# Performance work log

Hardware: AMD Instinct MI355X
Metric: run time of the kernel (lower is better)

The kernel has to match this reference:

```python
import jax, jax.numpy as jnp
import numpy as np

N_NODES = 20000
N_EDGES = 320000
D = 128  # d_edge = d_node = d_global


def setup_inputs() -> dict:
    key = jax.random.key(0)
    ks = jax.random.split(key, 8)
    inv = lambda fan_in: 1.0 / np.sqrt(fan_in)
    return {
        "edge_attr": jax.random.normal(ks[0], (N_EDGES, D), dtype=jnp.float32),
        "node_attr": jax.random.normal(ks[1], (N_NODES, D), dtype=jnp.float32),
        "u": jax.random.normal(ks[2], (D,), dtype=jnp.float32),
        "senders": jax.random.randint(ks[3], (N_EDGES,), 0, N_NODES, dtype=jnp.int32),
        "receivers": jax.random.randint(ks[4], (N_EDGES,), 0, N_NODES, dtype=jnp.int32),
        "We": jax.random.normal(ks[5], (4 * D, D), dtype=jnp.float32) * inv(4 * D),
        "be": jnp.zeros((D,), dtype=jnp.float32),
        "Wv": jax.random.normal(ks[6], (3 * D, D), dtype=jnp.float32) * inv(3 * D),
        "bv": jnp.zeros((D,), dtype=jnp.float32),
        "Wu": jax.random.normal(ks[7], (3 * D, D), dtype=jnp.float32) * inv(3 * D),
        "bu": jnp.zeros((D,), dtype=jnp.float32),
    }


def reference(edge_attr, node_attr, u, senders, receivers, We, be, Wv, bv, Wu, bu):
    E = edge_attr.shape[0]
    N = node_attr.shape[0]
    u_e = jnp.broadcast_to(u, (E, u.shape[0]))
    u_v = jnp.broadcast_to(u, (N, u.shape[0]))

    # Edge block: phi_e(e, v_r, v_s, u) -- gather endpoint features per edge
    e_in = jnp.concatenate(
        [edge_attr, node_attr[receivers], node_attr[senders], u_e], axis=-1
    )  # [E, 4D]
    e_new = jax.nn.relu(e_in @ We + be)  # [E, D]

    # rho_ev: sum incoming edges per receiver node (scatter-add)
    aggr_e = jax.ops.segment_sum(e_new, receivers, num_segments=N)  # [N, D]

    # Node block: phi_v(aggr_e, v, u)
    v_in = jnp.concatenate([aggr_e, node_attr, u_v], axis=-1)  # [N, 3D]
    v_new = jax.nn.relu(v_in @ Wv + bv)  # [N, D]

    # Global block: rho_eu / rho_vu = mean, phi_u(aggr_e, aggr_v, u)
    aggr_e_u = jnp.mean(e_new, axis=0)
    aggr_v_u = jnp.mean(v_new, axis=0)
    u_in = jnp.concatenate([aggr_e_u, aggr_v_u, u], axis=-1)  # [3D]
    u_new = jax.nn.relu(u_in @ Wu + bu)  # [D]

    return e_new, v_new, u_new
```

## Files before the change

### kernel.cpp

```cpp
#include <hip/hip_runtime.h>
#include <hip/hip_bf16.h>


#define NN 20000
#define NE 320000
#define DD 128
#define SAS 136
#define SBS 136
#define NBLK 512
#define NTILE 5000

#define BAR_LDS() asm volatile("s_waitcnt lgkmcnt(0)\n\ts_barrier" ::: "memory")

typedef unsigned short u16;
typedef __attribute__((ext_vector_type(8))) short bf16x8;
typedef __attribute__((ext_vector_type(4))) float f32x4;

__device__ __forceinline__ float b2f(unsigned short h) {
  return __uint_as_float(((unsigned int)h) << 16);
}
__device__ __forceinline__ unsigned short f2b(float f) {
  unsigned int u = __float_as_uint(f);
  unsigned int r = (u + 0x7fffu + ((u >> 16) & 1u)) >> 16;
  return (unsigned short)r;
}
__device__ __forceinline__ unsigned int addpk(unsigned int a, unsigned int b) {
  float lo = __uint_as_float(a << 16) + __uint_as_float(b << 16);
  float hi = __uint_as_float(a & 0xffff0000u) + __uint_as_float(b & 0xffff0000u);
  return (unsigned int)f2b(lo) | (((unsigned int)f2b(hi)) << 16);
}

__device__ __forceinline__ void mfma_core(const u16* sA, const u16* sBT,
                                          int lane, int w, f32x4 acc[4][2]) {
  int r15 = lane & 15;
  int koff = (lane >> 4) * 8;
#pragma unroll
  for (int k0 = 0; k0 < DD; k0 += 32) {
    bf16x8 a[4], b[2];
#pragma unroll
    for (int mt = 0; mt < 4; ++mt)
      a[mt] = *(const bf16x8*)&sA[(mt * 16 + r15) * SAS + k0 + koff];
#pragma unroll
    for (int nt = 0; nt < 2; ++nt)
      b[nt] = *(const bf16x8*)&sBT[(w * 32 + nt * 16 + r15) * SBS + k0 + koff];
#pragma unroll
    for (int mt = 0; mt < 4; ++mt)
#pragma unroll
      for (int nt = 0; nt < 2; ++nt)
        acc[mt][nt] = __builtin_amdgcn_mfma_f32_16x16x32_bf16(
            a[mt], b[nt], acc[mt][nt], 0, 0, 0);
  }
}

__device__ __forceinline__ void stage_w(u16* sBT, const u16* wsrc, int tid) {
  const uint4* ws = (const uint4*)wsrc;
  for (int i = tid; i < DD * DD / 8; i += 256) {
    int n = i >> 4, kk = (i & 15) * 8;
    *(uint4*)&sBT[n * SBS + kk] = ws[i];
  }
}

__global__ __launch_bounds__(256) void k_setup(const int* recv, int* counts,
                                               const float* We, const float* Wv,
                                               const float* u, const float* be,
                                               const float* bv, u16* wt,
                                               float* ce, float* cv) {
  __shared__ float su[DD];
  int b = blockIdx.x, tid = threadIdx.x;
  if (b < 1250) {
    atomicAdd(&counts[recv[b * 256 + tid]], 1);
  } else if (b < 1255) {
    int m = b - 1250;
    const float* W = (m == 0)   ? We
                     : (m == 1) ? We + 128 * DD
                     : (m == 2) ? We + 256 * DD
                     : (m == 3) ? Wv + 128 * DD
                                : Wv;
    u16* o = wt + (size_t)m * DD * DD;
    for (int i = tid; i < DD * DD; i += 256) {
      int k = i >> 7, n = i & 127;
      o[n * DD + k] = f2b(W[i]);
    }
  } else {
    if (tid < DD) su[tid] = u[tid];
    __syncthreads();
    if (tid < DD) {
      float a = be[tid], c = bv[tid];
      for (int k = 0; k < DD; ++k) {
        a = fmaf(su[k], We[(384 + k) * DD + tid], a);
        c = fmaf(su[k], Wv[(256 + k) * DD + tid], c);
      }
      ce[tid] = a;
      cv[tid] = c;
    }
  }
}

__global__ void k_scan(const int* counts, int* rowptr, int* cursor) {
  __shared__ int wsum[16];
  __shared__ int carry;
  int tid = threadIdx.x;
  int lane = tid & 63, wv = tid >> 6;
  if (tid == 0) carry = 0;
  __syncthreads();
  for (int base = 0; base < NN; base += 1024) {
    int i = base + tid;
    int v = (i < NN) ? counts[i] : 0;
    int x = v;
    for (int off = 1; off < 64; off <<= 1) {
      int t = __shfl_up(x, off);
      if (lane >= off) x += t;
    }
    if (lane == 63) wsum[wv] = x;
    __syncthreads();
    if (wv == 0 && lane < 16) {
      int y = wsum[lane];
      for (int off = 1; off < 16; off <<= 1) {
        int t = __shfl_up(y, off);
        if (lane >= off) y += t;
      }
      wsum[lane] = y;
    }
    __syncthreads();
    int woff = (wv > 0) ? wsum[wv - 1] : 0;
    int excl = carry + woff + (x - v);
    if (i < NN) {
      rowptr[i] = excl;
      cursor[i] = excl;
    }
    __syncthreads();
    if (tid == 0) carry += wsum[15];
    __syncthreads();
  }
  if (tid == 0) rowptr[NN] = carry;
}

__global__ __launch_bounds__(256) void k_mid(const int* recv, int* cursor,
                                             int* elist, const float* node_attr,
                                             const u16* wt, u16* P) {
  __shared__ __align__(16) u16 sA[64 * SAS];
  __shared__ __align__(16) u16 sBT[DD * SBS];
  int b = blockIdx.x, tid = threadIdx.x;
  if (b < 1250) {
    int e = b * 256 + tid;
    int slot = atomicAdd(&cursor[recv[e]], 1);
    elist[slot] = e;
    return;
  }
  int g = b - 1250;
  int n0 = (g / 3) * 64;
  int sel = g % 3;
  stage_w(sBT, wt + (size_t)(1 + sel) * DD * DD, tid);
  for (int i = tid; i < 64 * DD / 4; i += 256) {
    int rr = i >> 5, cc = (i & 31) * 4;
    float4 a4 = (n0 + rr < NN)
                    ? ((const float4*)node_attr)[(size_t)(n0 + rr) * 32 + (i & 31)]
                    : make_float4(0, 0, 0, 0);
    ushort4 h;
    h.x = f2b(a4.x); h.y = f2b(a4.y); h.z = f2b(a4.z); h.w = f2b(a4.w);
    *(ushort4*)&sA[rr * SAS + cc] = h;
  }
  __syncthreads();
  int lane = tid & 63, w = tid >> 6;
  int c15 = lane & 15, quad = lane >> 4;
  int col0 = w * 32 + c15, col1 = col0 + 16;
  f32x4 acc[4][2] = {};
  mfma_core(sA, sBT, lane, w, acc);
#pragma unroll
  for (int mt = 0; mt < 4; ++mt)
#pragma unroll
    for (int r = 0; r < 4; ++r) {
      int n = n0 + mt * 16 + quad * 4 + r;
      if (n < NN) {
        u16* o = &P[(size_t)n * 384 + sel * 128];
        o[col0] = f2b(acc[mt][0][r]);
        o[col1] = f2b(acc[mt][1][r]);
      }
    }
}

__global__ __launch_bounds__(512, 4) void k_edge(const float* edge_attr,
                                                 const u16* wt, const int* elist,
                                                 const int* recv, const int* send,
                                                 const u16* P, const float* ce,
                                                 float* e_out, float* aggr,
                                                 float* sum_e) {
  __shared__ __align__(16) u16 sA[64 * SAS];
  __shared__ __align__(16) u16 sPQ[64 * SAS];
  __shared__ int sEid[64], sRecv[64], sSend[64];
  int tid = threadIdx.x;
  int lane = tid & 63, w = tid >> 6;
  int r15 = lane & 15, quad = lane >> 4;
  int koff = quad * 8;
  int col0 = w * 16 + r15;
  int myrow = tid >> 5;
  int mycol = (tid & 31) * 4;
  int grow = tid >> 4;
  int gch = tid & 15;

  bf16x8 breg[4];
#pragma unroll
  for (int kk = 0; kk < 4; ++kk)
    breg[kk] =
        *(const bf16x8*)&wt[(size_t)(w * 16 + r15) * DD + kk * 32 + koff];
  float ce0 = ce[col0];

  float4 areg[4];
  int eid4[4];
  int eidN = 0, rcN = 0, sdN = 0;
  int t = blockIdx.x;

  {
    int base = t * 64;
#pragma unroll
    for (int j = 0; j < 4; ++j) eid4[j] = elist[base + myrow + 16 * j];
    if (tid < 64) {
      eidN = elist[base + tid];
      rcN = recv[eidN];
      sdN = send[eidN];
    }
#pragma unroll
    for (int j = 0; j < 4; ++j)
      areg[j] = *(const float4*)&edge_attr[(size_t)eid4[j] * DD + mycol];
  }
  float colsum = 0.f;
  bool first = true;

  for (; t < NTILE; t += NBLK) {
    if (!first) BAR_LDS();
    first = false;
#pragma unroll
    for (int j = 0; j < 4; ++j) {
      ushort4 h;
      h.x = f2b(areg[j].x); h.y = f2b(areg[j].y);
      h.z = f2b(areg[j].z); h.w = f2b(areg[j].w);
      *(ushort4*)&sA[(myrow + 16 * j) * SAS + mycol] = h;
    }
    if (tid < 64) {
      sEid[tid] = eidN;
      sRecv[tid] = rcN;
      sSend[tid] = sdN;
    }
    BAR_LDS();

    uint4 q1[2], q2[2];
#pragma unroll
    for (int j = 0; j < 2; ++j) {
      int row = grow + 32 * j;
      q1[j] = *((const uint4*)&P[(size_t)sRecv[row] * 384] + gch);
      q2[j] = *((const uint4*)&P[(size_t)sSend[row] * 384 + 128] + gch);
    }
    int tn = t + NBLK;
    if (tn < NTILE) {
      int base = tn * 64;
#pragma unroll
      for (int j = 0; j < 4; ++j) eid4[j] = elist[base + myrow + 16 * j];
      if (tid < 64) eidN = elist[base + tid];
    }

    f32x4 acc[4] = {};
#pragma unroll
    for (int kk = 0; kk < 4; ++kk) {
      bf16x8 a[4];
#pragma unroll
      for (int mt = 0; mt < 4; ++mt)
        a[mt] = *(const bf16x8*)&sA[(mt * 16 + r15) * SAS + kk * 32 + koff];
#pragma unroll
      for (int mt = 0; mt < 4; ++mt)
        acc[mt] = __builtin_amdgcn_mfma_f32_16x16x32_bf16(a[mt], breg[kk],
                                                          acc[mt], 0, 0, 0);
    }
    if (tn < NTILE) {
      if (tid < 64) {
        rcN = recv[eidN];
        sdN = send[eidN];
      }
#pragma unroll
      for (int j = 0; j < 4; ++j)
        areg[j] = *(const float4*)&edge_attr[(size_t)eid4[j] * DD + mycol];
    }
#pragma unroll
    for (int j = 0; j < 2; ++j) {
      int row = grow + 32 * j;
      uint4 o;
      o.x = addpk(q1[j].x, q2[j].x);
      o.y = addpk(q1[j].y, q2[j].y);
      o.z = addpk(q1[j].z, q2[j].z);
      o.w = addpk(q1[j].w, q2[j].w);
      *(uint4*)&sPQ[row * SAS + gch * 8] = o;
    }
    BAR_LDS();

#pragma unroll
    for (int mt = 0; mt < 4; ++mt)
#pragma unroll
      for (int r = 0; r < 4; ++r) {
        int m = mt * 16 + quad * 4 + r;
        float v = fmaxf(acc[mt][r] + b2f(sPQ[m * SAS + col0]) + ce0, 0.f);
        sA[m * SAS + col0] = f2b(v);
      }
    BAR_LDS();

    if (tid < 256) {
      int col = tid & 127, half = tid >> 7;
      int r0 = half * 32;
      float run = 0.f;
      int prev = sRecv[r0];
      for (int r = r0; r < r0 + 32; ++r) {
        int cur = sRecv[r];
        float v = b2f(sA[r * SAS + col]);
        if (cur != prev) {
          atomicAdd(&aggr[(size_t)prev * DD + col], run);
          run = 0.f;
          prev = cur;
        }
        run += v;
        colsum += v;
      }
      atomicAdd(&aggr[(size_t)prev * DD + col], run);
    } else {
      int tt = tid - 256;
#pragma unroll
      for (int j = 0; j < 4; ++j) {
        int i = tt + 256 * j;
        int row = i >> 4, ch = (i & 15) * 8;
        uint4 qq = *(const uint4*)&sA[row * SAS + ch];
        float4 f0, f1;
        f0.x = b2f((u16)(qq.x & 0xffff)); f0.y = b2f((u16)(qq.x >> 16));
        f0.z = b2f((u16)(qq.y & 0xffff)); f0.w = b2f((u16)(qq.y >> 16));
        f1.x = b2f((u16)(qq.z & 0xffff)); f1.y = b2f((u16)(qq.z >> 16));
        f1.z = b2f((u16)(qq.w & 0xffff)); f1.w = b2f((u16)(qq.w >> 16));
        float* dst = &e_out[(size_t)sEid[row] * DD + ch];
        *(float4*)dst = f0;
        *(float4*)(dst + 4) = f1;
      }
    }
  }
  if (tid < 256) atomicAdd(&sum_e[tid & 127], colsum);
}

__global__ __launch_bounds__(256) void k_node(const float* aggr, const u16* wt,
                                              const u16* P, const float* cv,
                                              float* v_out, float* sum_v) {
  __shared__ __align__(16) u16 sA[64 * SAS];
  __shared__ __align__(16) u16 sBT[DD * SBS];
  __shared__ float sCol[DD];
  int tid = threadIdx.x;
  int n0 = blockIdx.x * 64;
  stage_w(sBT, wt + (size_t)4 * DD * DD, tid);
  for (int i = tid; i < 64 * DD / 4; i += 256) {
    int rr = i >> 5, cc = (i & 31) * 4;
    float4 a4 = (n0 + rr < NN)
                    ? ((const float4*)aggr)[(size_t)(n0 + rr) * 32 + (i & 31)]
                    : make_float4(0, 0, 0, 0);
    ushort4 h;
    h.x = f2b(a4.x); h.y = f2b(a4.y); h.z = f2b(a4.z); h.w = f2b(a4.w);
    *(ushort4*)&sA[rr * SAS + cc] = h;
  }
  if (tid < DD) sCol[tid] = 0.f;
  __syncthreads();
  int lane = tid & 63, w = tid >> 6;
  f32x4 acc[4][2] = {};
  mfma_core(sA, sBT, lane, w, acc);
  int c15 = lane & 15, quad = lane >> 4;
  int col0 = w * 32 + c15, col1 = col0 + 16;
  float cv0 = cv[col0], cv1 = cv[col1];
  float cs0 = 0.f, cs1 = 0.f;
#pragma unroll
  for (int mt = 0; mt < 4; ++mt)
#pragma unroll
    for (int r = 0; r < 4; ++r) {
      int n = n0 + mt * 16 + quad * 4 + r;
      if (n < NN) {
        const u16* pv = &P[(size_t)n * 384 + 256];
        float v0 = fmaxf(acc[mt][0][r] + b2f(pv[col0]) + cv0, 0.f);
        float v1 = fmaxf(acc[mt][1][r] + b2f(pv[col1]) + cv1, 0.f);
        size_t ob = (size_t)n * DD;
        v_out[ob + col0] = v0;
        v_out[ob + col1] = v1;
        cs0 += v0;
        cs1 += v1;
      }
    }
  atomicAdd(&sCol[col0], cs0);
  atomicAdd(&sCol[col1], cs1);
  __syncthreads();
  if (tid < DD) atomicAdd(&sum_v[tid], sCol[tid]);
}

__global__ void k_global(const float* sumbuf, const float* u, const float* Wu,
                         const float* bu, float* out) {
  __shared__ float sin_[384];
  int j = threadIdx.x;
  sin_[j] = sumbuf[j] * (1.0f / (float)NE);
  sin_[128 + j] = sumbuf[128 + j] * (1.0f / (float)NN);
  sin_[256 + j] = u[j];
  __syncthreads();
  float a = bu[j];
  for (int k = 0; k < 384; ++k) a = fmaf(sin_[k], Wu[k * DD + j], a);
  out[j] = fmaxf(a, 0.f);
}

extern "C" void kernel_launch(void* const* d_in, const int* in_sizes, int n_in,
                              void* d_out, int out_size, void* d_ws,
                              size_t ws_size, hipStream_t stream) {
  const float* edge_attr = (const float*)d_in[0];
  const float* node_attr = (const float*)d_in[1];
  const float* u = (const float*)d_in[2];
  const int* senders = (const int*)d_in[3];
  const int* receivers = (const int*)d_in[4];
  const float* We = (const float*)d_in[5];
  const float* be = (const float*)d_in[6];
  const float* Wv = (const float*)d_in[7];
  const float* bv = (const float*)d_in[8];
  const float* Wu = (const float*)d_in[9];
  const float* bu = (const float*)d_in[10];

  float* e_out = (float*)d_out;
  float* v_out = e_out + (size_t)NE * DD;
  float* u_out = v_out + (size_t)NN * DD;

  int* counts = (int*)d_ws;
  float* sumbuf = (float*)d_ws + NN;
  float* aggr = (float*)d_ws + NN + 256;
  int* rowptr = (int*)d_ws + NN + 256 + NN * DD;
  int* cursor = rowptr + NN + 1;
  int* elist = cursor + NN;
  size_t off = (size_t)(NN + 256 + NN * DD + (NN + 1) + NN + NE);
  off = (off + 3) & ~(size_t)3;
  u16* wt = (u16*)((float*)d_ws + off);
  u16* P = wt + (size_t)5 * DD * DD;
  float* ce = (float*)(P + (size_t)NN * 384);
  float* cv = ce + 128;

  hipMemsetAsync(d_ws, 0, (size_t)(NN + 256 + NN * DD) * 4, stream);
  k_setup<<<1256, 256, 0, stream>>>(receivers, counts, We, Wv, u, be, bv, wt,
                                    ce, cv);
  k_scan<<<1, 1024, 0, stream>>>(counts, rowptr, cursor);
  k_mid<<<1250 + 939, 256, 0, stream>>>(receivers, cursor, elist, node_attr,
                                        wt, P);
  k_edge<<<NBLK, 512, 0, stream>>>(edge_attr, wt, elist, receivers, senders, P,
                                   ce, e_out, aggr, sumbuf);
  k_node<<<(NN + 63) / 64, 256, 0, stream>>>(aggr, wt, P, cv, v_out,
                                             sumbuf + 128);
  k_global<<<1, 128, 0, stream>>>(sumbuf, u, Wu, bu, u_out);
}
```

Measured before the change: 494.5 us.

## Deepen edge-kernel prefetch pipeline with double-buffered metadata and early P gathers

The edge kernel now keeps edge indices, receiver/sender metadata and the gathered P rows one or two tiles ahead, using double-buffered shared arrays for per-tile metadata. This way the dependent index→recv/send→P gather chain is spread across iterations instead of stalling inside one. The setup kernel's weight transpose now goes through shared memory so the global stores are coalesced. The barrier macro also switches to the builtin barrier. In exchange, more registers stay live across iterations, which may cut occupancy under the 512-thread launch bound.

```diff
diff --git a/kernel.cpp b/kernel.cpp
--- a/kernel.cpp
+++ b/kernel.cpp
@@ -10,7 +10,11 @@
 #define NBLK 512
 #define NTILE 5000
 
-#define BAR_LDS() asm volatile("s_waitcnt lgkmcnt(0)\n\ts_barrier" ::: "memory")
+#define BAR_LDS()                                        \
+  do {                                                   \
+    asm volatile("s_waitcnt lgkmcnt(0)" ::: "memory");   \
+    __builtin_amdgcn_s_barrier();                        \
+  } while (0)
 
 typedef unsigned short u16;
 typedef __attribute__((ext_vector_type(8))) short bf16x8;
@@ -66,6 +70,7 @@
                                                const float* bv, u16* wt,
                                                float* ce, float* cv) {
   __shared__ float su[DD];
+  __shared__ __align__(16) u16 sT[DD * SAS];
   int b = blockIdx.x, tid = threadIdx.x;
   if (b < 1250) {
     atomicAdd(&counts[recv[b * 256 + tid]], 1);
@@ -76,10 +81,15 @@
                      : (m == 2) ? We + 256 * DD
                      : (m == 3) ? Wv + 128 * DD
                                 : Wv;
-    u16* o = wt + (size_t)m * DD * DD;
     for (int i = tid; i < DD * DD; i += 256) {
       int k = i >> 7, n = i & 127;
-      o[n * DD + k] = f2b(W[i]);
+      sT[n * SAS + k] = f2b(W[i]);
+    }
+    __syncthreads();
+    u16* o = wt + (size_t)m * DD * DD;
+    for (int i = tid; i < DD * DD / 8; i += 256) {
+      int n = i >> 4, c = (i & 15) * 8;
+      *(uint4*)&o[n * DD + c] = *(const uint4*)&sT[n * SAS + c];
     }
   } else {
     if (tid < DD) su[tid] = u[tid];
@@ -187,7 +197,7 @@
                                                  float* sum_e) {
   __shared__ __align__(16) u16 sA[64 * SAS];
   __shared__ __align__(16) u16 sPQ[64 * SAS];
-  __shared__ int sEid[64], sRecv[64], sSend[64];
+  __shared__ int sEid[2][64], sRecv[2][64], sSend[2][64];
   int tid = threadIdx.x;
   int lane = tid & 63, w = tid >> 6;
   int r15 = lane & 15, quad = lane >> 4;
@@ -206,27 +216,49 @@
   float ce0 = ce[col0];
 
   float4 areg[4];
-  int eid4[4];
-  int eidN = 0, rcN = 0, sdN = 0;
+  int eid4R[4];
+  int metaE = 0, metaRc = 0, metaSd = 0;
+  int eidNN = 0;
+  uint4 q1[2], q2[2];
+
   int t = blockIdx.x;
-
   {
     int base = t * 64;
-#pragma unroll
-    for (int j = 0; j < 4; ++j) eid4[j] = elist[base + myrow + 16 * j];
     if (tid < 64) {
-      eidN = elist[base + tid];
-      rcN = recv[eidN];
-      sdN = send[eidN];
-    }
+      int e = elist[base + tid];
+      metaE = e; metaRc = recv[e]; metaSd = send[e];
+      sEid[0][tid] = e; sRecv[0][tid] = metaRc; sSend[0][tid] = metaSd;
+    }
+#pragma unroll
+    for (int j = 0; j < 4; ++j) eid4R[j] = elist[base + myrow + 16 * j];
 #pragma unroll
     for (int j = 0; j < 4; ++j)
-      areg[j] = *(const float4*)&edge_attr[(size_t)eid4[j] * DD + mycol];
+      areg[j] = *(const float4*)&edge_attr[(size_t)eid4R[j] * DD + mycol];
+    BAR_LDS();
+#pragma unroll
+    for (int j = 0; j < 2; ++j) {
+      int row = grow + 32 * j;
+      q1[j] = *((const uint4*)&P[(size_t)sRecv[0][row] * 384] + gch);
+      q2[j] = *((const uint4*)&P[(size_t)sSend[0][row] * 384 + 128] + gch);
+    }
+    int tn = t + NBLK;
+    if (tn < NTILE) {
+      int bn = tn * 64;
+#pragma unroll
+      for (int j = 0; j < 4; ++j) eid4R[j] = elist[bn + myrow + 16 * j];
+      if (tid < 64) {
+        int e = elist[bn + tid];
+        metaE = e; metaRc = recv[e]; metaSd = send[e];
+      }
+    }
   }
   float colsum = 0.f;
+  int cur = 0;
   bool first = true;
 
   for (; t < NTILE; t += NBLK) {
+    int tn = t + NBLK, tnn = tn + NBLK;
+    int nxt = cur ^ 1;
     if (!first) BAR_LDS();
     first = false;
 #pragma unroll
@@ -236,27 +268,23 @@
       h.z = f2b(areg[j].z); h.w = f2b(areg[j].w);
       *(ushort4*)&sA[(myrow + 16 * j) * SAS + mycol] = h;
     }
-    if (tid < 64) {
-      sEid[tid] = eidN;
-      sRecv[tid] = rcN;
-      sSend[tid] = sdN;
+    if (tn < NTILE) {
+#pragma unroll
+      for (int j = 0; j < 4; ++j)
+        areg[j] = *(const float4*)&edge_attr[(size_t)eid4R[j] * DD + mycol];
+    }
+    if (tnn < NTILE) {
+      int bn = tnn * 64;
+#pragma unroll
+      for (int j = 0; j < 4; ++j) eid4R[j] = elist[bn + myrow + 16 * j];
+      if (tid < 64) eidNN = elist[bn + tid];
+    }
+    if (tn < NTILE && tid < 64) {
+      sEid[nxt][tid] = metaE;
+      sRecv[nxt][tid] = metaRc;
+      sSend[nxt][tid] = metaSd;
     }
     BAR_LDS();
-
-    uint4 q1[2], q2[2];
-#pragma unroll
-    for (int j = 0; j < 2; ++j) {
-      int row = grow + 32 * j;
-      q1[j] = *((const uint4*)&P[(size_t)sRecv[row] * 384] + gch);
-      q2[j] = *((const uint4*)&P[(size_t)sSend[row] * 384 + 128] + gch);
-    }
-    int tn = t + NBLK;
-    if (tn < NTILE) {
-      int base = tn * 64;
-#pragma unroll
-      for (int j = 0; j < 4; ++j) eid4[j] = elist[base + myrow + 16 * j];
-      if (tid < 64) eidN = elist[base + tid];
-    }
 
     f32x4 acc[4] = {};
 #pragma unroll
@@ -269,15 +297,6 @@
       for (int mt = 0; mt < 4; ++mt)
         acc[mt] = __builtin_amdgcn_mfma_f32_16x16x32_bf16(a[mt], breg[kk],
                                                           acc[mt], 0, 0, 0);
-    }
-    if (tn < NTILE) {
-      if (tid < 64) {
-        rcN = recv[eidN];
-        sdN = send[eidN];
-      }
-#pragma unroll
-      for (int j = 0; j < 4; ++j)
-        areg[j] = *(const float4*)&edge_attr[(size_t)eid4[j] * DD + mycol];
     }
 #pragma unroll
     for (int j = 0; j < 2; ++j) {
@@ -289,6 +308,14 @@
       o.w = addpk(q1[j].w, q2[j].w);
       *(uint4*)&sPQ[row * SAS + gch * 8] = o;
     }
+    if (tn < NTILE) {
+#pragma unroll
+      for (int j = 0; j < 2; ++j) {
+        int row = grow + 32 * j;
+        q1[j] = *((const uint4*)&P[(size_t)sRecv[nxt][row] * 384] + gch);
+        q2[j] = *((const uint4*)&P[(size_t)sSend[nxt][row] * 384 + 128] + gch);
+      }
+    }
     BAR_LDS();
 
 #pragma unroll
@@ -299,20 +326,25 @@
         float v = fmaxf(acc[mt][r] + b2f(sPQ[m * SAS + col0]) + ce0, 0.f);
         sA[m * SAS + col0] = f2b(v);
       }
+    if (tnn < NTILE && tid < 64) {
+      metaE = eidNN;
+      metaRc = recv[eidNN];
+      metaSd = send[eidNN];
+    }
     BAR_LDS();
 
     if (tid < 256) {
       int col = tid & 127, half = tid >> 7;
       int r0 = half * 32;
       float run = 0.f;
-      int prev = sRecv[r0];
+      int prev = sRecv[cur][r0];
       for (int r = r0; r < r0 + 32; ++r) {
-        int cur = sRecv[r];
+        int cr = sRecv[cur][r];
         float v = b2f(sA[r * SAS + col]);
-        if (cur != prev) {
+        if (cr != prev) {
           atomicAdd(&aggr[(size_t)prev * DD + col], run);
           run = 0.f;
-          prev = cur;
+          prev = cr;
         }
         run += v;
         colsum += v;
@@ -330,11 +362,12 @@
         f0.z = b2f((u16)(qq.y & 0xffff)); f0.w = b2f((u16)(qq.y >> 16));
         f1.x = b2f((u16)(qq.z & 0xffff)); f1.y = b2f((u16)(qq.z >> 16));
         f1.z = b2f((u16)(qq.w & 0xffff)); f1.w = b2f((u16)(qq.w >> 16));
-        float* dst = &e_out[(size_t)sEid[row] * DD + ch];
+        float* dst = &e_out[(size_t)sEid[cur][row] * DD + ch];
         *(float4*)dst = f0;
         *(float4*)(dst + 4) = f1;
       }
     }
+    cur ^= 1;
   }
   if (tid < 256) atomicAdd(&sum_e[tid & 127], colsum);
 }
```

Result: slower. 506.4 us (+2.4%).
